# Kernel optimization log

Hardware: AMD Instinct MI355X
Metric: run time of the kernel (lower is better)

Reference implementation:

```python
import jax, jax.numpy as jnp
import numpy as np

B, C, N, D, H, NC = 128, 9, 2048, 192, 384, 18  # batch, in_chans, time, embed, mlp_hidden, classes


def setup_inputs() -> dict:
    key = jax.random.key(0)
    ks = jax.random.split(key, 18)
    rn = lambda k, sh, s=0.02: jax.random.normal(k, sh, dtype=jnp.float32) * s
    return {
        "x": jax.random.normal(ks[0], (B, C, N), dtype=jnp.float32),
        "conv_w": rn(ks[1], (D, C, 3)),
        "conv_b": jnp.zeros((D,), jnp.float32),
        "pos_embed": jnp.zeros((1, N, D), jnp.float32),
        "qkv_w": rn(ks[2], (3 * D, D)),
        "qkv_b": jnp.zeros((3 * D,), jnp.float32),
        "proj_w": rn(ks[3], (D, D)),
        "proj_b": jnp.zeros((D,), jnp.float32),
        "ln1_g": jnp.ones((D,), jnp.float32),
        "ln1_b": jnp.zeros((D,), jnp.float32),
        "mlp_w1": rn(ks[4], (H, D)),
        "mlp_b1": jnp.zeros((H,), jnp.float32),
        "mlp_w2": rn(ks[5], (D, H)),
        "mlp_b2": jnp.zeros((D,), jnp.float32),
        "ln2_g": jnp.ones((D,), jnp.float32),
        "ln2_b": jnp.zeros((D,), jnp.float32),
        "head_w": rn(ks[6], (NC, D)),
        "head_b": jnp.zeros((NC,), jnp.float32),
    }


def _ln(x, g, b, eps=1e-5):
    m = x.mean(-1, keepdims=True)
    v = ((x - m) ** 2).mean(-1, keepdims=True)
    return (x - m) * jax.lax.rsqrt(v + eps) * g + b


def reference(x, conv_w, conv_b, pos_embed, qkv_w, qkv_b, proj_w, proj_b,
              ln1_g, ln1_b, mlp_w1, mlp_b1, mlp_w2, mlp_b2, ln2_g, ln2_b,
              head_w, head_b):
    # patch embed: Conv1d(C->D, k=3, pad=1), then [B, N, D]
    h = jax.lax.conv_general_dilated(
        x, conv_w, window_strides=(1,), padding=[(1, 1)],
        dimension_numbers=("NCH", "OIH", "NCH")) + conv_b[None, :, None]
    h = jnp.transpose(h, (0, 2, 1)) + pos_embed  # [B, N, D]

    # linear (Performer-style) attention with ReLU feature maps
    hn = _ln(h, ln1_g, ln1_b)
    qkv = hn @ qkv_w.T + qkv_b  # [B, N, 3D]
    q, k, v = jnp.split(qkv, 3, axis=-1)
    q = jax.nn.relu(q)
    k = jax.nn.relu(k)
    kv = jnp.einsum("bnd,bne->bde", k, v)       # [B, D, D]
    num = jnp.einsum("bnd,bde->bne", q, kv)      # [B, N, D]
    # NOTE: original sums q over BOTH token and feature dims -> scalar per batch
    denom = q.sum(axis=(1, 2))[:, None, None]
    attn = num / (denom + 1e-6)
    h = h + attn @ proj_w.T + proj_b

    # MLP block (exact GELU, as torch nn.GELU default)
    hn2 = _ln(h, ln2_g, ln2_b)
    m = jax.nn.gelu(hn2 @ mlp_w1.T + mlp_b1, approximate=False)
    h = h + m @ mlp_w2.T + mlp_b2

    # head: AdaptiveAvgPool1d(1) over time, then Linear
    pooled = h.mean(axis=1)  # [B, D]
    return pooled @ head_w.T + head_b  # [B, NC]
```

## Files before the change

### kernel.cpp

```cpp
#include <hip/hip_runtime.h>
#include <cmath>

#define B_   128
#define C_   9
#define N_   2048
#define D_   192
#define H_   384
#define NC_  18

typedef unsigned short ushort_t;
typedef __attribute__((ext_vector_type(8))) __bf16 bf16x8;
typedef __attribute__((ext_vector_type(8))) short short8;
typedef __attribute__((ext_vector_type(16))) float f32x16;

__device__ __forceinline__ ushort_t f2bf(float x) {
    unsigned u = __float_as_uint(x);
    return (ushort_t)((u + 0x7fffu + ((u >> 16) & 1u)) >> 16);
}
__device__ __forceinline__ float bf2f(ushort_t h) {
    return __uint_as_float(((unsigned)h) << 16);
}
__device__ __forceinline__ bf16x8 ldfrag(const ushort_t* p) {
    short8 s = *(const short8*)p;
    return __builtin_bit_cast(bf16x8, s);
}

__global__ __launch_bounds__(192) void conv_ln_k(
    const float* __restrict__ x, const float* __restrict__ w,
    const float* __restrict__ cb, const float* __restrict__ pos,
    const float* __restrict__ lng, const float* __restrict__ lnb,
    float* __restrict__ h, ushort_t* __restrict__ oh, ushort_t* __restrict__ ol)
{
    const int n0 = blockIdx.x * 64;
    const int b  = blockIdx.y;
    const int d  = threadIdx.x;

    __shared__ float xs[C_][66];
    __shared__ float tile[64][193];
    __shared__ float ps[64][3], pq[64][3];
    __shared__ float mm[64], rr[64];

    for (int e = threadIdx.x; e < C_ * 66; e += 192) {
        int c = e / 66, i = e % 66;
        int n = n0 - 1 + i;
        xs[c][i] = (n >= 0 && n < N_) ? x[((size_t)b * C_ + c) * N_ + n] : 0.f;
    }
    float wr[C_][3];
#pragma unroll
    for (int c = 0; c < C_; ++c)
#pragma unroll
        for (int t = 0; t < 3; ++t) wr[c][t] = w[(d * C_ + c) * 3 + t];
    const float bias = cb[d];
    __syncthreads();

    for (int i = 0; i < 64; ++i) {
        float acc = bias + pos[(size_t)(n0 + i) * D_ + d];
#pragma unroll
        for (int c = 0; c < C_; ++c)
#pragma unroll
            for (int t = 0; t < 3; ++t) acc += xs[c][i + t] * wr[c][t];
        tile[i][d] = acc;
    }
    __syncthreads();

    {
        int row = threadIdx.x & 63, part = threadIdx.x >> 6;
        float s = 0.f, q = 0.f;
        const float* tr = &tile[row][part * 64];
#pragma unroll 8
        for (int j = 0; j < 64; ++j) { float v = tr[j]; s += v; q += v * v; }
        ps[row][part] = s; pq[row][part] = q;
    }
    __syncthreads();
    if (threadIdx.x < 64) {
        int r = threadIdx.x;
        float s = ps[r][0] + ps[r][1] + ps[r][2];
        float q = pq[r][0] + pq[r][1] + pq[r][2];
        float m = s * (1.f / D_);
        mm[r] = m;
        rr[r] = rsqrtf(q * (1.f / D_) - m * m + 1e-5f);
    }
    __syncthreads();
    {
        const float gd = lng[d], bd = lnb[d];
        for (int i = 0; i < 64; ++i) {
            float v = tile[i][d];
            size_t idx = ((size_t)b * N_ + n0 + i) * D_ + d;
            h[idx] = v;
            float nv = (v - mm[i]) * rr[i] * gd + bd;
            ushort_t hb = f2bf(nv);
            oh[idx] = hb;
            ol[idx] = f2bf(nv - bf2f(hb));
        }
    }
}

__global__ __launch_bounds__(256) void splitw_k(
    const float* __restrict__ w, ushort_t* __restrict__ hi, ushort_t* __restrict__ lo, int n)
{
    int i = blockIdx.x * 256 + threadIdx.x;
    if (i < n) {
        float v = w[i];
        ushort_t hb = f2bf(v);
        hi[i] = hb;
        lo[i] = f2bf(v - bf2f(hb));
    }
}

template <int EPI, int BM, int NBY>
__global__ __launch_bounds__(256) void mgemm(
    const ushort_t* __restrict__ Ah, const ushort_t* __restrict__ Al, int K,
    const ushort_t* __restrict__ Wh, const ushort_t* __restrict__ Wl,
    const float* __restrict__ bias, float* __restrict__ dsum,
    const float* __restrict__ lng, const float* __restrict__ lnb,
    ushort_t* __restrict__ oh, ushort_t* __restrict__ ol,
    ushort_t* __restrict__ kTh, ushort_t* __restrict__ kTl,
    ushort_t* __restrict__ vTh, ushort_t* __restrict__ vTl,
    float* __restrict__ facc)
{
    extern __shared__ ushort_t smem[];
    constexpr int MI     = BM / 64;
    constexpr int APL    = BM * 32;
    constexpr int AK     = BM * 8;
    constexpr int AELEMS = BM * 64;
    constexpr int BUFE   = AELEMS + 12288;
    constexpr int ACH    = 8 * MI;
    constexpr int NCH    = ACH + 24;

    const int tid  = threadIdx.x;
    const int lane = tid & 63;
    const int l5   = lane >> 5;
    const int wid  = tid >> 6;
    const int wr = wid >> 1, wc = wid & 1;

    int bx, by;
    if (EPI == 4) { bx = blockIdx.x; by = 0; }
    else {
        int gmx = gridDim.x / NBY;
        int xx = blockIdx.x & 7, ii = blockIdx.x >> 3;
        by = ii % NBY;
        bx = xx * (gmx >> 3) + ii / NBY;
    }
    const int m0 = bx * BM;

    size_t wbase = 0;
    if (EPI == 0 || EPI == 1) wbase = (size_t)by * 192 * K;
    else if (EPI == 3) wbase = (size_t)(m0 >> 11) * D_ * D_;
    else if (EPI == 4) wbase = (size_t)(bx / 3) * 192 * (size_t)K;
    const ushort_t* Whp = Wh + wbase;
    const ushort_t* Wlp = Wl + wbase;

    int kbeg = 0, kend = K;
    if (EPI == 4) { int seg = K / gridDim.z; kbeg = blockIdx.z * seg; kend = kbeg + seg; }

    auto stage = [&](int buf, int k0) {
        const int base = buf * BUFE;
#pragma unroll
        for (int i = 0; i < NCH / 4; ++i) {
            int c = wid + i * 4;
            const ushort_t* src;
            int dst;
            if (c < ACH) {
                int koct = c & 3, tt = c >> 2;
                int plane = tt & 1, rb = tt >> 1;
                const ushort_t* ap = plane ? Al : Ah;
                src = ap + (size_t)(m0 + rb * 64 + lane) * K + k0 + koct * 8;
                dst = plane * APL + koct * AK + rb * 512;
            } else {
                int c2 = c - ACH;
                int koct = c2 & 3, tt = c2 >> 2;
                int plane = tt & 1, rb = tt >> 1;
                const ushort_t* wp = plane ? Wlp : Whp;
                src = wp + (size_t)(rb * 64 + lane) * K + k0 + koct * 8;
                dst = AELEMS + plane * 6144 + koct * 1536 + rb * 512;
            }
            __builtin_amdgcn_global_load_lds(
                (const __attribute__((address_space(1))) void*)src,
                (__attribute__((address_space(3))) void*)(smem + base + dst),
                16, 0, 0);
        }
    };

    f32x16 acc[MI][3] = {};

    const int nt = (kend - kbeg) / 32;
    stage(0, kbeg);
    __syncthreads();
    int cur = 0;
    for (int t = 0; t < nt; ++t) {
        if (t + 1 < nt) stage(cur ^ 1, kbeg + (t + 1) * 32);
        const ushort_t* bb = smem + cur * BUFE;
#pragma unroll
        for (int kh = 0; kh < 2; ++kh) {
            bf16x8 ah[MI], al[MI];
#pragma unroll
            for (int mi = 0; mi < MI; ++mi) {
                int ao = (kh * 2 + l5) * AK + (wr * (BM / 2) + mi * 32 + (lane & 31)) * 8;
                ah[mi] = ldfrag(bb + ao);
                al[mi] = ldfrag(bb + APL + ao);
            }
#pragma unroll
            for (int tn = 0; tn < 3; ++tn) {
                int wo = AELEMS + (kh * 2 + l5) * 1536 + (wc * 96 + tn * 32 + (lane & 31)) * 8;
                bf16x8 wh = ldfrag(bb + wo);
                bf16x8 wl = ldfrag(bb + wo + 6144);
#pragma unroll
                for (int mi = 0; mi < MI; ++mi) {
                    acc[mi][tn] = __builtin_amdgcn_mfma_f32_32x32x16_bf16(ah[mi], wh, acc[mi][tn], 0, 0, 0);
                    acc[mi][tn] = __builtin_amdgcn_mfma_f32_32x32x16_bf16(ah[mi], wl, acc[mi][tn], 0, 0, 0);
                    acc[mi][tn] = __builtin_amdgcn_mfma_f32_32x32x16_bf16(al[mi], wh, acc[mi][tn], 0, 0, 0);
                }
            }
        }
        __syncthreads();
        cur ^= 1;
    }

    const int cb = wc * 96 + (lane & 31);

    if (EPI == 0) {
        if (by == 0) {
            float qsum = 0.f;
#pragma unroll
            for (int mi = 0; mi < MI; ++mi) {
                const int rb0 = m0 + wr * (BM / 2) + mi * 32 + 4 * l5;
#pragma unroll
                for (int tn = 0; tn < 3; ++tn) {
                    const int col = cb + tn * 32;
                    const float bv = bias[col];
#pragma unroll
                    for (int r = 0; r < 16; ++r) {
                        int row = rb0 + (r & 3) + 8 * (r >> 2);
                        float v = fmaxf(acc[mi][tn][r] + bv, 0.f);
                        qsum += v;
                        ushort_t hb = f2bf(v);
                        oh[(size_t)row * D_ + col] = hb;
                        ol[(size_t)row * D_ + col] = f2bf(v - bf2f(hb));
                    }
                }
            }
            __syncthreads();
            float* red = (float*)smem;
            red[tid] = qsum;
            __syncthreads();
            for (int o = 128; o > 0; o >>= 1) {
                if (tid < o) red[tid] += red[tid + o];
                __syncthreads();
            }
            if (tid == 0) dsum[(m0 >> 11) * 16 + ((m0 >> 7) & 15)] = red[0];
        } else {
            ushort_t* dsth = (by == 1) ? kTh : vTh;
            ushort_t* dstl = (by == 1) ? kTl : vTl;
            constexpr int STR = BM + 8;
#pragma unroll
            for (int plane = 0; plane < 2; ++plane) {
                __syncthreads();
#pragma unroll
                for (int mi = 0; mi < MI; ++mi) {
                    const int rl0 = wr * (BM / 2) + mi * 32 + 4 * l5;
#pragma unroll
                    for (int tn = 0; tn < 3; ++tn) {
                        const int col = cb + tn * 32;
                        const float bv = bias[by * 192 + col];
#pragma unroll
                        for (int r = 0; r < 16; ++r) {
                            int rowl = rl0 + (r & 3) + 8 * (r >> 2);
                            float v = acc[mi][tn][r] + bv;
                            if (by == 1) v = fmaxf(v, 0.f);
                            ushort_t hb = f2bf(v);
                            smem[col * STR + rowl] = plane ? f2bf(v - bf2f(hb)) : hb;
                        }
                    }
                }
                __syncthreads();
                if (tid < 192) {
                    ushort_t* dst = plane ? dstl : dsth;
                    size_t gbase = ((size_t)(m0 >> 11) * 192 + tid) * (size_t)N_ + (m0 & 2047);
#pragma unroll
                    for (int i2 = 0; i2 < BM / 8; ++i2)
                        *(uint4*)(dst + gbase + i2 * 8) = *(const uint4*)&smem[tid * STR + i2 * 8];
                }
            }
        }
    } else if (EPI == 1) {
#pragma unroll
        for (int mi = 0; mi < MI; ++mi) {
            const int rb0 = m0 + wr * (BM / 2) + mi * 32 + 4 * l5;
#pragma unroll
            for (int tn = 0; tn < 3; ++tn) {
                const int colg = by * 192 + cb + tn * 32;
                const float bv = bias[colg];
#pragma unroll
                for (int r = 0; r < 16; ++r) {
                    int row = rb0 + (r & 3) + 8 * (r >> 2);
                    float v = acc[mi][tn][r] + bv;
                    float gv = 0.5f * v * (1.f + erff(v * 0.70710678118654752f));
                    ushort_t hb = f2bf(gv);
                    oh[(size_t)row * H_ + colg] = hb;
                    ol[(size_t)row * H_ + colg] = f2bf(gv - bf2f(hb));
                }
            }
        }
    } else if (EPI == 2) {
        float tsum[3] = {0.f, 0.f, 0.f};
#pragma unroll
        for (int mi = 0; mi < MI; ++mi) {
            const int rb0 = m0 + wr * (BM / 2) + mi * 32 + 4 * l5;
#pragma unroll
            for (int tn = 0; tn < 3; ++tn) {
                const int col = cb + tn * 32;
                const float bv = bias[col];
#pragma unroll
                for (int r = 0; r < 16; ++r) {
                    int row = rb0 + (r & 3) + 8 * (r >> 2);
                    float v = facc[(size_t)row * D_ + col] + acc[mi][tn][r] + bv;
                    facc[(size_t)row * D_ + col] = v;
                    tsum[tn] += v;
                }
            }
        }
#pragma unroll
        for (int tn = 0; tn < 3; ++tn) {
            float t = tsum[tn];
            t += __shfl_xor(t, 32);
            if (l5 == 0) atomicAdd(&dsum[(size_t)(m0 >> 11) * D_ + cb + tn * 32], t);
        }
    } else if (EPI == 3) {
        float ds = 0.f;
        const float* dp = dsum + (m0 >> 11) * 16;
#pragma unroll
        for (int j = 0; j < 16; ++j) ds += dp[j];
        const float s = 1.f / (ds + 1e-6f);
#pragma unroll
        for (int mi = 0; mi < MI; ++mi) {
            const int rb0 = m0 + wr * (BM / 2) + mi * 32 + 4 * l5;
#pragma unroll
            for (int tn = 0; tn < 3; ++tn) {
                const int col = cb + tn * 32;
                const float bv = bias[col];
#pragma unroll
                for (int r = 0; r < 16; ++r) {
                    int row = rb0 + (r & 3) + 8 * (r >> 2);
                    float v = facc[(size_t)row * D_ + col] + acc[mi][tn][r] * s + bv;
                    facc[(size_t)row * D_ + col] = v;
                    acc[mi][tn][r] = v;
                }
            }
        }
        float* ls = (float*)smem;
        float* lq = ls + 256;
        float* lm = lq + 256;
        float* lr = lm + 128;
#pragma unroll
        for (int mi = 0; mi < MI; ++mi) {
#pragma unroll
            for (int r = 0; r < 16; ++r) {
                float pv = acc[mi][0][r] + acc[mi][1][r] + acc[mi][2][r];
                float qv = acc[mi][0][r] * acc[mi][0][r] + acc[mi][1][r] * acc[mi][1][r]
                         + acc[mi][2][r] * acc[mi][2][r];
#pragma unroll
                for (int off = 1; off <= 16; off <<= 1) {
                    pv += __shfl_xor(pv, off);
                    qv += __shfl_xor(qv, off);
                }
                if ((lane & 31) == 0) {
                    int rl = wr * 64 + mi * 32 + 4 * l5 + (r & 3) + 8 * (r >> 2);
                    ls[rl * 2 + wc] = pv;
                    lq[rl * 2 + wc] = qv;
                }
            }
        }
        __syncthreads();
        if (tid < 128) {
            float sv = ls[tid * 2] + ls[tid * 2 + 1];
            float qv = lq[tid * 2] + lq[tid * 2 + 1];
            float mv = sv * (1.f / D_);
            lm[tid] = mv;
            lr[tid] = rsqrtf(qv * (1.f / D_) - mv * mv + 1e-5f);
        }
        __syncthreads();
#pragma unroll
        for (int mi = 0; mi < MI; ++mi) {
#pragma unroll
            for (int tn = 0; tn < 3; ++tn) {
                const int col = cb + tn * 32;
                const float gv = lng[col], bv2 = lnb[col];
#pragma unroll
                for (int r = 0; r < 16; ++r) {
                    int rl = wr * 64 + mi * 32 + 4 * l5 + (r & 3) + 8 * (r >> 2);
                    float nv = (acc[mi][tn][r] - lm[rl]) * lr[rl] * gv + bv2;
                    ushort_t hb = f2bf(nv);
                    size_t idx = (size_t)(m0 + rl) * D_ + col;
                    oh[idx] = hb;
                    ol[idx] = f2bf(nv - bf2f(hb));
                }
            }
        }
    } else if (EPI == 4) {
        float* fz = facc + (size_t)blockIdx.z * ((size_t)(gridDim.x / 3) * D_ * D_);
#pragma unroll
        for (int mi = 0; mi < MI; ++mi) {
            const int rb0 = m0 + wr * (BM / 2) + mi * 32 + 4 * l5;
#pragma unroll
            for (int tn = 0; tn < 3; ++tn) {
                const int col = cb + tn * 32;
#pragma unroll
                for (int r = 0; r < 16; ++r) {
                    int row = rb0 + (r & 3) + 8 * (r >> 2);
                    fz[(size_t)row * D_ + col] = acc[mi][tn][r];
                }
            }
        }
    }
}

__global__ __launch_bounds__(256) void kv2_k(
    const float* __restrict__ pw, const float* __restrict__ kvs, size_t span,
    ushort_t* __restrict__ oh, ushort_t* __restrict__ ol)
{
    __shared__ float As[16][68];
    __shared__ float Ws[16][68];
    const int tid = threadIdx.x;
    const int tx = tid & 15, ty = tid >> 4;
    const int m0 = blockIdx.x * 64;
    const int n0 = blockIdx.y * 64;
    const int b = blockIdx.z;
    const int lm = tid >> 2;
    const int lk = (tid & 3) * 4;

    float acc[4][4] = {};
    for (int k0 = 0; k0 < D_; k0 += 16) {
        float4 av = *(const float4*)(pw + (size_t)(m0 + lm) * D_ + k0 + lk);
        As[lk + 0][lm] = av.x; As[lk + 1][lm] = av.y;
        As[lk + 2][lm] = av.z; As[lk + 3][lm] = av.w;
        const float* base = kvs + (size_t)b * D_ * D_ + (size_t)(n0 + lm) * D_ + k0 + lk;
        float4 wv = {0.f, 0.f, 0.f, 0.f};
#pragma unroll
        for (int z = 0; z < 8; ++z) {
            float4 t = *(const float4*)(base + z * span);
            wv.x += t.x; wv.y += t.y; wv.z += t.z; wv.w += t.w;
        }
        Ws[lk + 0][lm] = wv.x; Ws[lk + 1][lm] = wv.y;
        Ws[lk + 2][lm] = wv.z; Ws[lk + 3][lm] = wv.w;
        __syncthreads();
#pragma unroll
        for (int kk = 0; kk < 16; ++kk) {
            float4 a4 = *(const float4*)&As[kk][ty * 4];
            float4 w4 = *(const float4*)&Ws[kk][tx * 4];
            float a[4] = {a4.x, a4.y, a4.z, a4.w};
            float w[4] = {w4.x, w4.y, w4.z, w4.w};
#pragma unroll
            for (int i = 0; i < 4; ++i)
#pragma unroll
                for (int j = 0; j < 4; ++j) acc[i][j] += a[i] * w[j];
        }
        __syncthreads();
    }
#pragma unroll
    for (int i = 0; i < 4; ++i) {
        ushort_t hb[4], lb[4];
#pragma unroll
        for (int j = 0; j < 4; ++j) {
            float v = acc[i][j];
            hb[j] = f2bf(v);
            lb[j] = f2bf(v - bf2f(hb[j]));
        }
        size_t base = (size_t)b * D_ * D_ + (size_t)(m0 + ty * 4 + i) * D_ + n0 + tx * 4;
        *(uint2*)&oh[base] = make_uint2((unsigned)hb[0] | ((unsigned)hb[1] << 16),
                                        (unsigned)hb[2] | ((unsigned)hb[3] << 16));
        *(uint2*)&ol[base] = make_uint2((unsigned)lb[0] | ((unsigned)lb[1] << 16),
                                        (unsigned)lb[2] | ((unsigned)lb[3] << 16));
    }
}

__global__ __launch_bounds__(192) void head_k(
    const float* __restrict__ pooled, const float* __restrict__ hw,
    const float* __restrict__ hb, float* __restrict__ out)
{
    const int b = blockIdx.x, d = threadIdx.x;
    __shared__ float p[D_];
    p[d] = pooled[(size_t)b * D_ + d] * (1.f / N_);
    __syncthreads();
    if (d < NC_) {
        float acc = hb[d];
        for (int e = 0; e < D_; ++e) acc += p[e] * hw[d * D_ + e];
        out[b * NC_ + d] = acc;
    }
}

extern "C" void kernel_launch(void* const* d_in, const int* in_sizes, int n_in,
                              void* d_out, int out_size, void* d_ws, size_t ws_size,
                              hipStream_t stream) {
    (void)in_sizes; (void)n_in; (void)out_size;

    const float* x      = (const float*)d_in[0];
    const float* conv_w = (const float*)d_in[1];
    const float* conv_b = (const float*)d_in[2];
    const float* pos    = (const float*)d_in[3];
    const float* qkv_w  = (const float*)d_in[4];
    const float* qkv_b  = (const float*)d_in[5];
    const float* proj_w = (const float*)d_in[6];
    const float* proj_b = (const float*)d_in[7];
    const float* ln1_g  = (const float*)d_in[8];
    const float* ln1_b  = (const float*)d_in[9];
    const float* mlp_w1 = (const float*)d_in[10];
    const float* mlp_b1 = (const float*)d_in[11];
    const float* mlp_w2 = (const float*)d_in[12];
    const float* mlp_b2 = (const float*)d_in[13];
    const float* ln2_g  = (const float*)d_in[14];
    const float* ln2_b  = (const float*)d_in[15];
    const float* head_w = (const float*)d_in[16];
    const float* head_b = (const float*)d_in[17];
    float* out = (float*)d_out;

    const size_t perB =
        (size_t)N_ * D_ * 4 +
        (size_t)N_ * D_ * 2 * 2 +
        (size_t)N_ * D_ * 2 * 2 +
        (size_t)N_ * D_ * 2 * 4 +
        (size_t)D_ * D_ * 2 * 2 +
        8192;
    const size_t fixedW = 2ull * (576 * 192 + 384 * 192 + 192 * 384) * 2 + 65536;
    int BC = B_;
    while (BC > 1 && fixedW + (size_t)BC * perB > ws_size) BC >>= 1;
    const int nchunks = B_ / BC;
    const size_t rows = (size_t)BC * N_;

    char* p = (char*)d_ws;
    auto alloc = [&](size_t bytes) -> char* {
        char* r = p;
        p += (bytes + 255) & ~(size_t)255;
        return r;
    };
    ushort_t* qw_hi = (ushort_t*)alloc(576 * 192 * 2);
    ushort_t* qw_lo = (ushort_t*)alloc(576 * 192 * 2);
    ushort_t* w1_hi = (ushort_t*)alloc(384 * 192 * 2);
    ushort_t* w1_lo = (ushort_t*)alloc(384 * 192 * 2);
    ushort_t* w2_hi = (ushort_t*)alloc(192 * 384 * 2);
    ushort_t* w2_lo = (ushort_t*)alloc(192 * 384 * 2);

    const size_t szPl = rows * D_ * 2;
    float*    h      = (float*)alloc(rows * D_ * 4);
    ushort_t* hn_hi  = (ushort_t*)alloc(szPl);
    ushort_t* hn_lo  = (ushort_t*)alloc(szPl);
    ushort_t* q_hi   = (ushort_t*)alloc(szPl);
    ushort_t* q_lo   = (ushort_t*)alloc(szPl);
    ushort_t* kT_hi  = (ushort_t*)alloc(szPl);
    ushort_t* kT_lo  = (ushort_t*)alloc(szPl);
    ushort_t* vT_hi  = (ushort_t*)alloc(szPl);
    ushort_t* vT_lo  = (ushort_t*)alloc(szPl);
    ushort_t* kv2t_h = (ushort_t*)alloc((size_t)BC * D_ * D_ * 2);
    ushort_t* kv2t_l = (ushort_t*)alloc((size_t)BC * D_ * D_ * 2);
    float*    dsum   = (float*)alloc((size_t)BC * 16 * 4);
    float*    pooled = (float*)alloc((size_t)BC * D_ * 4);
    ushort_t* m_hi   = kT_hi;
    ushort_t* m_lo   = vT_hi;
    float*    kvs    = (float*)hn_hi;
    const size_t kvspan = (size_t)BC * D_ * D_;

    splitw_k<<<(576 * 192 + 255) / 256, 256, 0, stream>>>(qkv_w, qw_hi, qw_lo, 576 * 192);
    splitw_k<<<(384 * 192 + 255) / 256, 256, 0, stream>>>(mlp_w1, w1_hi, w1_lo, 384 * 192);
    splitw_k<<<(192 * 384 + 255) / 256, 256, 0, stream>>>(mlp_w2, w2_hi, w2_lo, 192 * 384);

    const int gm = (int)(rows / 128);
    const size_t SHT = (size_t)(128 * 64 + 12288) * 2 * 2;
    const size_t SH4 = (size_t)(64 * 64 + 12288) * 2 * 2;

    for (int ch = 0; ch < nchunks; ++ch) {
        const int b0 = ch * BC;
        const float* xc = x + (size_t)b0 * C_ * N_;

        hipMemsetAsync(pooled, 0, (size_t)BC * D_ * 4, stream);

        conv_ln_k<<<dim3(N_ / 64, BC), 192, 0, stream>>>(
            xc, conv_w, conv_b, pos, ln1_g, ln1_b, h, hn_hi, hn_lo);
        mgemm<0, 128, 3><<<gm * 3, 256, SHT, stream>>>(
            hn_hi, hn_lo, D_, qw_hi, qw_lo, qkv_b, dsum, nullptr, nullptr,
            q_hi, q_lo, kT_hi, kT_lo, vT_hi, vT_lo, nullptr);
        mgemm<4, 64, 1><<<dim3(BC * 3, 1, 8), 256, SH4, stream>>>(
            kT_hi, kT_lo, N_, vT_hi, vT_lo, nullptr, nullptr, nullptr, nullptr,
            nullptr, nullptr, nullptr, nullptr, nullptr, nullptr, kvs);
        kv2_k<<<dim3(3, 3, BC), 256, 0, stream>>>(proj_w, kvs, kvspan, kv2t_h, kv2t_l);
        mgemm<3, 128, 1><<<gm, 256, SHT, stream>>>(
            q_hi, q_lo, D_, kv2t_h, kv2t_l, proj_b, dsum, ln2_g, ln2_b,
            hn_hi, hn_lo, nullptr, nullptr, nullptr, nullptr, h);
        mgemm<1, 128, 2><<<gm * 2, 256, SHT, stream>>>(
            hn_hi, hn_lo, D_, w1_hi, w1_lo, mlp_b1, nullptr, nullptr, nullptr,
            m_hi, m_lo, nullptr, nullptr, nullptr, nullptr, nullptr);
        mgemm<2, 128, 1><<<gm, 256, SHT, stream>>>(
            m_hi, m_lo, H_, w2_hi, w2_lo, mlp_b2, pooled, nullptr, nullptr,
            nullptr, nullptr, nullptr, nullptr, nullptr, nullptr, h);
        head_k<<<BC, 192, 0, stream>>>(pooled, head_w, head_b, out + (size_t)b0 * NC_);
    }
}
```

Baseline: 1.718 ms.

## Load pre-packed weight fragments straight from global memory, bypassing LDS in GEMMs

Result: slower. 2.014 ms (+17.3%).

```diff
diff --git a/kernel.cpp b/kernel.cpp
--- a/kernel.cpp
+++ b/kernel.cpp
@@ -95,20 +95,23 @@
     }
 }
 
-__global__ __launch_bounds__(256) void splitw_k(
-    const float* __restrict__ w, ushort_t* __restrict__ hi, ushort_t* __restrict__ lo, int n)
+__global__ __launch_bounds__(256) void splitw_pack_k(
+    const float* __restrict__ w, ushort_t* __restrict__ hi, ushort_t* __restrict__ lo,
+    int NW, int K)
 {
     int i = blockIdx.x * 256 + threadIdx.x;
-    if (i < n) {
-        float v = w[i];
-        ushort_t hb = f2bf(v);
-        hi[i] = hb;
-        lo[i] = f2bf(v - bf2f(hb));
-    }
+    if (i >= NW * K) return;
+    int row = i / K, k = i % K;
+    int g = row / 192, c = row % 192;
+    float v = w[i];
+    ushort_t hb = f2bf(v);
+    size_t o = (size_t)g * K * 192 + (size_t)(k >> 4) * 3072 + (size_t)c * 16 + (k & 15);
+    hi[o] = hb;
+    lo[o] = f2bf(v - bf2f(hb));
 }
 
 template <int EPI, int BM, int NBY>
-__global__ __launch_bounds__(256) void mgemm(
+__global__ __launch_bounds__(256, 3) void mgemm(
     const ushort_t* __restrict__ Ah, const ushort_t* __restrict__ Al, int K,
     const ushort_t* __restrict__ Wh, const ushort_t* __restrict__ Wl,
     const float* __restrict__ bias, float* __restrict__ dsum,
@@ -119,13 +122,10 @@
     float* __restrict__ facc)
 {
     extern __shared__ ushort_t smem[];
-    constexpr int MI     = BM / 64;
-    constexpr int APL    = BM * 32;
-    constexpr int AK     = BM * 8;
-    constexpr int AELEMS = BM * 64;
-    constexpr int BUFE   = AELEMS + 12288;
-    constexpr int ACH    = 8 * MI;
-    constexpr int NCH    = ACH + 24;
+    constexpr int MI   = BM / 64;
+    constexpr int APL  = BM * 32;
+    constexpr int BUFE = BM * 64;
+    constexpr int ACH  = 8 * MI;
 
     const int tid  = threadIdx.x;
     const int lane = tid & 63;
@@ -134,8 +134,7 @@
     const int wr = wid >> 1, wc = wid & 1;
 
     int bx, by;
-    if (EPI == 4) { bx = blockIdx.x; by = 0; }
-    else {
+    {
         int gmx = gridDim.x / NBY;
         int xx = blockIdx.x & 7, ii = blockIdx.x >> 3;
         by = ii % NBY;
@@ -146,71 +145,62 @@
     size_t wbase = 0;
     if (EPI == 0 || EPI == 1) wbase = (size_t)by * 192 * K;
     else if (EPI == 3) wbase = (size_t)(m0 >> 11) * D_ * D_;
-    else if (EPI == 4) wbase = (size_t)(bx / 3) * 192 * (size_t)K;
     const ushort_t* Whp = Wh + wbase;
     const ushort_t* Wlp = Wl + wbase;
 
-    int kbeg = 0, kend = K;
-    if (EPI == 4) { int seg = K / gridDim.z; kbeg = blockIdx.z * seg; kend = kbeg + seg; }
-
     auto stage = [&](int buf, int k0) {
         const int base = buf * BUFE;
 #pragma unroll
-        for (int i = 0; i < NCH / 4; ++i) {
+        for (int i = 0; i < ACH / 4; ++i) {
             int c = wid + i * 4;
-            const ushort_t* src;
-            int dst;
-            if (c < ACH) {
-                int koct = c & 3, tt = c >> 2;
-                int plane = tt & 1, rb = tt >> 1;
-                const ushort_t* ap = plane ? Al : Ah;
-                src = ap + (size_t)(m0 + rb * 64 + lane) * K + k0 + koct * 8;
-                dst = plane * APL + koct * AK + rb * 512;
-            } else {
-                int c2 = c - ACH;
-                int koct = c2 & 3, tt = c2 >> 2;
-                int plane = tt & 1, rb = tt >> 1;
-                const ushort_t* wp = plane ? Wlp : Whp;
-                src = wp + (size_t)(rb * 64 + lane) * K + k0 + koct * 8;
-                dst = AELEMS + plane * 6144 + koct * 1536 + rb * 512;
-            }
+            int koct = c & 3, tt = c >> 2;
+            int plane = tt & 1, rb = tt >> 1;
+            const ushort_t* ap = plane ? Al : Ah;
+            const ushort_t* src = ap + (size_t)(m0 + rb * 64 + lane) * K + k0 + koct * 8;
+            int dst = base + plane * APL + koct * (BM * 8) + rb * 512;
             __builtin_amdgcn_global_load_lds(
                 (const __attribute__((address_space(1))) void*)src,
-                (__attribute__((address_space(3))) void*)(smem + base + dst),
+                (__attribute__((address_space(3))) void*)(smem + dst),
                 16, 0, 0);
         }
     };
 
     f32x16 acc[MI][3] = {};
 
-    const int nt = (kend - kbeg) / 32;
-    stage(0, kbeg);
+    const int nt = K / 32;
+    stage(0, 0);
     __syncthreads();
     int cur = 0;
     for (int t = 0; t < nt; ++t) {
-        if (t + 1 < nt) stage(cur ^ 1, kbeg + (t + 1) * 32);
+        bf16x8 wf[2][3][2];
+#pragma unroll
+        for (int kh = 0; kh < 2; ++kh)
+#pragma unroll
+            for (int tn = 0; tn < 3; ++tn) {
+                size_t off = (size_t)(t * 2 + kh) * 3072
+                           + (size_t)(wc * 96 + tn * 32 + (lane & 31)) * 16 + l5 * 8;
+                wf[kh][tn][0] = ldfrag(Whp + off);
+                wf[kh][tn][1] = ldfrag(Wlp + off);
+            }
+        if (t + 1 < nt) stage(cur ^ 1, (t + 1) * 32);
         const ushort_t* bb = smem + cur * BUFE;
 #pragma unroll
         for (int kh = 0; kh < 2; ++kh) {
             bf16x8 ah[MI], al[MI];
 #pragma unroll
             for (int mi = 0; mi < MI; ++mi) {
-                int ao = (kh * 2 + l5) * AK + (wr * (BM / 2) + mi * 32 + (lane & 31)) * 8;
+                int ao = (kh * 2 + l5) * (BM * 8) + (wr * (BM / 2) + mi * 32 + (lane & 31)) * 8;
                 ah[mi] = ldfrag(bb + ao);
                 al[mi] = ldfrag(bb + APL + ao);
             }
 #pragma unroll
-            for (int tn = 0; tn < 3; ++tn) {
-                int wo = AELEMS + (kh * 2 + l5) * 1536 + (wc * 96 + tn * 32 + (lane & 31)) * 8;
-                bf16x8 wh = ldfrag(bb + wo);
-                bf16x8 wl = ldfrag(bb + wo + 6144);
+            for (int tn = 0; tn < 3; ++tn)
 #pragma unroll
                 for (int mi = 0; mi < MI; ++mi) {
-                    acc[mi][tn] = __builtin_amdgcn_mfma_f32_32x32x16_bf16(ah[mi], wh, acc[mi][tn], 0, 0, 0);
-                    acc[mi][tn] = __builtin_amdgcn_mfma_f32_32x32x16_bf16(ah[mi], wl, acc[mi][tn], 0, 0, 0);
-                    acc[mi][tn] = __builtin_amdgcn_mfma_f32_32x32x16_bf16(al[mi], wh, acc[mi][tn], 0, 0, 0);
-                }
-            }
+                    acc[mi][tn] = __builtin_amdgcn_mfma_f32_32x32x16_bf16(ah[mi], wf[kh][tn][0], acc[mi][tn], 0, 0, 0);
+                    acc[mi][tn] = __builtin_amdgcn_mfma_f32_32x32x16_bf16(ah[mi], wf[kh][tn][1], acc[mi][tn], 0, 0, 0);
+                    acc[mi][tn] = __builtin_amdgcn_mfma_f32_32x32x16_bf16(al[mi], wf[kh][tn][0], acc[mi][tn], 0, 0, 0);
+                }
         }
         __syncthreads();
         cur ^= 1;
@@ -247,7 +237,7 @@
                 if (tid < o) red[tid] += red[tid + o];
                 __syncthreads();
             }
-            if (tid == 0) dsum[(m0 >> 11) * 16 + ((m0 >> 7) & 15)] = red[0];
+            if (tid == 0) dsum[(m0 >> 11) * 16 + (bx & 15)] = red[0];
         } else {
             ushort_t* dsth = (by == 1) ? kTh : vTh;
             ushort_t* dstl = (by == 1) ? kTl : vTl;
@@ -396,20 +386,101 @@
                 }
             }
         }
-    } else if (EPI == 4) {
-        float* fz = facc + (size_t)blockIdx.z * ((size_t)(gridDim.x / 3) * D_ * D_);
-#pragma unroll
-        for (int mi = 0; mi < MI; ++mi) {
-            const int rb0 = m0 + wr * (BM / 2) + mi * 32 + 4 * l5;
+    }
+}
+
+__global__ __launch_bounds__(256) void mgemm_kv(
+    const ushort_t* __restrict__ Ah, const ushort_t* __restrict__ Al,
+    const ushort_t* __restrict__ Wh, const ushort_t* __restrict__ Wl,
+    float* __restrict__ facc, size_t span)
+{
+    extern __shared__ ushort_t smem[];
+    constexpr int BM = 64;
+    constexpr int APL = BM * 32, AK = BM * 8, AELEMS = BM * 64;
+    constexpr int BUFE = AELEMS + 12288;
+    constexpr int ACH = 8, NCH = ACH + 24;
+
+    const int tid  = threadIdx.x;
+    const int lane = tid & 63;
+    const int l5   = lane >> 5;
+    const int wid  = tid >> 6;
+    const int wr = wid >> 1, wc = wid & 1;
+    const int bx = blockIdx.x;
+    const int m0 = bx * BM;
+
+    const size_t wbase = (size_t)(bx / 3) * 192 * (size_t)N_;
+    const ushort_t* Whp = Wh + wbase;
+    const ushort_t* Wlp = Wl + wbase;
+
+    const int seg = N_ / gridDim.z;
+    const int kbeg = blockIdx.z * seg, kend = kbeg + seg;
+
+    auto stage = [&](int buf, int k0) {
+        const int base = buf * BUFE;
+#pragma unroll
+        for (int i = 0; i < NCH / 4; ++i) {
+            int c = wid + i * 4;
+            const ushort_t* src;
+            int dst;
+            if (c < ACH) {
+                int koct = c & 3, tt = c >> 2;
+                int plane = tt & 1;
+                const ushort_t* ap = plane ? Al : Ah;
+                src = ap + (size_t)(m0 + lane) * N_ + k0 + koct * 8;
+                dst = plane * APL + koct * AK;
+            } else {
+                int c2 = c - ACH;
+                int koct = c2 & 3, tt = c2 >> 2;
+                int plane = tt & 1, rb = tt >> 1;
+                const ushort_t* wp = plane ? Wlp : Whp;
+                src = wp + (size_t)(rb * 64 + lane) * N_ + k0 + koct * 8;
+                dst = AELEMS + plane * 6144 + koct * 1536 + rb * 512;
+            }
+            __builtin_amdgcn_global_load_lds(
+                (const __attribute__((address_space(1))) void*)src,
+                (__attribute__((address_space(3))) void*)(smem + base + dst),
+                16, 0, 0);
+        }
+    };
+
+    f32x16 acc[3] = {};
+
+    const int nt = (kend - kbeg) / 32;
+    stage(0, kbeg);
+    __syncthreads();
+    int cur = 0;
+    for (int t = 0; t < nt; ++t) {
+        if (t + 1 < nt) stage(cur ^ 1, kbeg + (t + 1) * 32);
+        const ushort_t* bb = smem + cur * BUFE;
+#pragma unroll
+        for (int kh = 0; kh < 2; ++kh) {
+            int ao = (kh * 2 + l5) * AK + (wr * 32 + (lane & 31)) * 8;
+            bf16x8 ah = ldfrag(bb + ao);
+            bf16x8 al = ldfrag(bb + APL + ao);
 #pragma unroll
             for (int tn = 0; tn < 3; ++tn) {
-                const int col = cb + tn * 32;
-#pragma unroll
-                for (int r = 0; r < 16; ++r) {
-                    int row = rb0 + (r & 3) + 8 * (r >> 2);
-                    fz[(size_t)row * D_ + col] = acc[mi][tn][r];
-                }
-            }
+                int wo = AELEMS + (kh * 2 + l5) * 1536 + (wc * 96 + tn * 32 + (lane & 31)) * 8;
+                bf16x8 wh = ldfrag(bb + wo);
+                bf16x8 wl = ldfrag(bb + wo + 6144);
+                acc[tn] = __builtin_amdgcn_mfma_f32_32x32x16_bf16(ah, wh, acc[tn], 0, 0, 0);
+                acc[tn] = __builtin_amdgcn_mfma_f32_32x32x16_bf16(ah, wl, acc[tn], 0, 0, 0);
+                acc[tn] = __builtin_amdgcn_mfma_f32_32x32x16_bf16(al, wh, acc[tn], 0, 0, 0);
+            }
+        }
+        __syncthreads();
+        cur ^= 1;
+    }
+
+    float* fz = facc + (size_t)blockIdx.z * span;
+    const int cb = wc * 96 + (lane & 31);
+    const int rb0 = m0 + wr * 32 + 4 * l5;
+#pragma unroll
+    for (int tn = 0; tn < 3; ++tn) {
+        const int col = cb + tn * 32;
+#pragma unroll
+        for (int r = 0; r < 16; ++r) {
+            int row = rb0 + (r & 3) + 8 * (r >> 2);
+            fz[(size_t)row * D_ + col] = acc[tn][r];
         }
     }
 }
@@ -456,6 +527,7 @@
         }
         __syncthreads();
     }
+    const int d0 = n0 + tx * 4;
 #pragma unroll
     for (int i = 0; i < 4; ++i) {
         ushort_t hb[4], lb[4];
@@ -465,11 +537,12 @@
             hb[j] = f2bf(v);
             lb[j] = f2bf(v - bf2f(hb[j]));
         }
-        size_t base = (size_t)b * D_ * D_ + (size_t)(m0 + ty * 4 + i) * D_ + n0 + tx * 4;
-        *(uint2*)&oh[base] = make_uint2((unsigned)hb[0] | ((unsigned)hb[1] << 16),
-                                        (unsigned)hb[2] | ((unsigned)hb[3] << 16));
-        *(uint2*)&ol[base] = make_uint2((unsigned)lb[0] | ((unsigned)lb[1] << 16),
-                                        (unsigned)lb[2] | ((unsigned)lb[3] << 16));
+        const int e = m0 + ty * 4 + i;
+        size_t off = (size_t)b * D_ * D_ + ((size_t)(d0 >> 4) * 192 + e) * 16 + (d0 & 15);
+        *(uint2*)&oh[off] = make_uint2((unsigned)hb[0] | ((unsigned)hb[1] << 16),
+                                       (unsigned)hb[2] | ((unsigned)hb[3] << 16));
+        *(uint2*)&ol[off] = make_uint2((unsigned)lb[0] | ((unsigned)lb[1] << 16),
+                                       (unsigned)lb[2] | ((unsigned)lb[3] << 16));
     }
 }
 
@@ -558,12 +631,13 @@
     float*    kvs    = (float*)hn_hi;
     const size_t kvspan = (size_t)BC * D_ * D_;
 
-    splitw_k<<<(576 * 192 + 255) / 256, 256, 0, stream>>>(qkv_w, qw_hi, qw_lo, 576 * 192);
-    splitw_k<<<(384 * 192 + 255) / 256, 256, 0, stream>>>(mlp_w1, w1_hi, w1_lo, 384 * 192);
-    splitw_k<<<(192 * 384 + 255) / 256, 256, 0, stream>>>(mlp_w2, w2_hi, w2_lo, 192 * 384);
+    splitw_pack_k<<<(576 * 192 + 255) / 256, 256, 0, stream>>>(qkv_w, qw_hi, qw_lo, 576, 192);
+    splitw_pack_k<<<(384 * 192 + 255) / 256, 256, 0, stream>>>(mlp_w1, w1_hi, w1_lo, 384, 192);
+    splitw_pack_k<<<(192 * 384 + 255) / 256, 256, 0, stream>>>(mlp_w2, w2_hi, w2_lo, 192, 384);
 
     const int gm = (int)(rows / 128);
-    const size_t SHT = (size_t)(128 * 64 + 12288) * 2 * 2;
+    const size_t SH0 = 192 * (128 + 8) * 2;
+    const size_t SHT = (size_t)128 * 64 * 2 * 2;
     const size_t SH4 = (size_t)(64 * 64 + 12288) * 2 * 2;
 
     for (int ch = 0; ch < nchunks; ++ch) {
@@ -574,12 +648,11 @@
 
         conv_ln_k<<<dim3(N_ / 64, BC), 192, 0, stream>>>(
             xc, conv_w, conv_b, pos, ln1_g, ln1_b, h, hn_hi, hn_lo);
-        mgemm<0, 128, 3><<<gm * 3, 256, SHT, stream>>>(
+        mgemm<0, 128, 3><<<gm * 3, 256, SH0, stream>>>(
             hn_hi, hn_lo, D_, qw_hi, qw_lo, qkv_b, dsum, nullptr, nullptr,
             q_hi, q_lo, kT_hi, kT_lo, vT_hi, vT_lo, nullptr);
-        mgemm<4, 64, 1><<<dim3(BC * 3, 1, 8), 256, SH4, stream>>>(
-            kT_hi, kT_lo, N_, vT_hi, vT_lo, nullptr, nullptr, nullptr, nullptr,
-            nullptr, nullptr, nullptr, nullptr, nullptr, nullptr, kvs);
+        mgemm_kv<<<dim3(BC * 3, 1, 8), 256, SH4, stream>>>(
+            kT_hi, kT_lo, vT_hi, vT_lo, kvs, kvspan);
         kv2_k<<<dim3(3, 3, BC), 256, 0, stream>>>(proj_w, kvs, kvspan, kv2t_h, kv2t_l);
         mgemm<3, 128, 1><<<gm, 256, SHT, stream>>>(
             q_hi, q_lo, D_, kv2t_h, kv2t_l, proj_b, dsum, ln2_g, ln2_b,
```
